# Kernel tuning notes

Measured on AMD Instinct MI355X. Metric: run time of the kernel, lower is better.

The kernel has to match this reference:

```python
import jax, jax.numpy as jnp
import numpy as np

EPS = 1e-7  # K.epsilon()
ROUTINGS = 3
NUM_CAPSULE = 32
DIM_CAPSULE = 64


def squash(x, axis=-1):
    # NOTE: faithful to the source: x / sqrt(sum(x^2) + eps) (no squash factor)
    s = jnp.sum(jnp.square(x), axis=axis, keepdims=True)
    return x / jnp.sqrt(s + EPS)


def setup_inputs() -> dict:
    key = jax.random.key(0)
    k1, k2 = jax.random.split(key)
    B, I, C = 32, 1024, 256
    u_vecs = jax.random.normal(k1, (B, I, C), dtype=jnp.float32)
    # glorot-ish scale for the capsule kernel (1x1 conv == matmul C -> N*D)
    W = jax.random.normal(k2, (C, NUM_CAPSULE * DIM_CAPSULE), dtype=jnp.float32) * 0.03
    return {"u_vecs": u_vecs, "W": W}


def reference(u_vecs, W):
    B, I, C = u_vecs.shape
    N, D = NUM_CAPSULE, DIM_CAPSULE
    # conv1d with kernel size 1 == matmul; reshape + permute to (B, N, I, D)
    u_hat = jnp.einsum('bic,ce->bie', u_vecs, W)  # (B, I, N*D)
    u_hat = u_hat.reshape(B, I, N, D).transpose(0, 2, 1, 3)  # (B, N, I, D)

    b = jnp.zeros((B, N, I), dtype=u_hat.dtype)
    outputs = None
    for i in range(ROUTINGS):
        c = jax.nn.softmax(b, axis=1)  # softmax over num_capsule axis
        outputs = squash(jnp.einsum('bni,bnid->bnd', c, u_hat))  # (B, N, D)
        if i < ROUTINGS - 1:
            b = jnp.einsum('bnd,bnid->bni', outputs, u_hat)
    return outputs
```

## Files before the change

### kernel.cpp

```cpp
#include <hip/hip_runtime.h>
#include <math.h>


constexpr int Bn = 32, In = 1024, Cn = 256, Nn = 32, Dn = 64, ND = 2048;

typedef __attribute__((ext_vector_type(8))) short bf16x8;
typedef __attribute__((ext_vector_type(4))) float f32x4;

__device__ __forceinline__ unsigned int packbf2(float a, float b) {
  unsigned int xa = __float_as_uint(a), xb = __float_as_uint(b);
  xa = (xa + 0x7fffu + ((xa >> 16) & 1u)) >> 16;
  xb = (xb + 0x7fffu + ((xb >> 16) & 1u)) >> 16;
  return xa | (xb << 16);
}
__device__ __forceinline__ unsigned short packbf1(float a) {
  unsigned int x = __float_as_uint(a);
  return (unsigned short)((x + 0x7fffu + ((x >> 16) & 1u)) >> 16);
}
__device__ __forceinline__ float bfu(unsigned short us) {
  return __uint_as_float((unsigned int)us << 16);
}

__global__ __launch_bounds__(256) void k_pre(
    const float* __restrict__ u, const float* __restrict__ W,
    float* __restrict__ psu, unsigned short* __restrict__ Wbf,
    unsigned short* __restrict__ WbfT, unsigned short* __restrict__ ub16,
    unsigned short* __restrict__ uT16) {
  const int z = blockIdx.x, tid = threadIdx.x;
  if (z < 1024) {
    int b = z >> 5, ch = z & 31;
    const float* up = u + ((size_t)(b * In + ch * 32)) * Cn + tid;
    unsigned short* ubp = ub16 + ((size_t)(b * In + ch * 32)) * Cn + tid;
    float s = 0.f;
    unsigned int q[16];
#pragma unroll
    for (int m = 0; m < 16; ++m) {
      float v0 = up[(size_t)(2 * m) * Cn];
      float v1 = up[(size_t)(2 * m + 1) * Cn];
      s += v0 + v1;
      ubp[(size_t)(2 * m) * Cn] = packbf1(v0);
      ubp[(size_t)(2 * m + 1) * Cn] = packbf1(v1);
      q[m] = packbf2(v0, v1);
    }
    psu[(size_t)z * Cn + tid] = s;
    unsigned short* tp = uT16 + ((size_t)(b * Cn + tid)) * In + ch * 32;
    *(uint4*)&tp[0]  = make_uint4(q[0], q[1], q[2], q[3]);
    *(uint4*)&tp[8]  = make_uint4(q[4], q[5], q[6], q[7]);
    *(uint4*)&tp[16] = make_uint4(q[8], q[9], q[10], q[11]);
    *(uint4*)&tp[24] = make_uint4(q[12], q[13], q[14], q[15]);
  } else if (z < 1152) {
    __shared__ float tile[64][65];
    int t = z - 1024;
    int x0 = (t & 31) * 64, y0 = (t >> 5) * 64;
    int lx = tid & 63, ly = tid >> 6;
#pragma unroll
    for (int k = 0; k < 16; ++k) {
      int y = ly + k * 4;
      tile[y][lx] = W[(size_t)(y0 + y) * ND + x0 + lx];
    }
    __syncthreads();
#pragma unroll
    for (int k = 0; k < 8; ++k) {
      int idx = tid + k * 256;
      int row = idx >> 5, cu = idx & 31;
      unsigned int v = packbf2(tile[2 * cu][row], tile[2 * cu + 1][row]);
      *(unsigned int*)&WbfT[(size_t)(x0 + row) * Cn + y0 + 2 * cu] = v;
    }
  } else {
    int zb = z - 1152;
    const float* src = W + (size_t)zb * 4096;
    unsigned short* dst = Wbf + (size_t)zb * 4096;
#pragma unroll
    for (int k = 0; k < 4; ++k) {
      int off = k * 1024 + tid * 4;
      const float4 v = *(const float4*)&src[off];
      *(uint2*)&dst[off] = make_uint2(packbf2(v.x, v.y), packbf2(v.z, v.w));
    }
  }
}

__global__ __launch_bounds__(512) void k_sst(
    const void* __restrict__ src, int srcBf16, long bS, long nS, long cS,
    float scale, const unsigned short* __restrict__ Wbf,
    const unsigned short* __restrict__ WbfT, unsigned short* __restrict__ tb,
    float* __restrict__ outp, int writeT) {
  int bn = blockIdx.x, b = bn >> 5, n = bn & 31;
  int tid = threadIdx.x;
  __shared__ float vs[Cn];
  __shared__ float ol[Dn];
  __shared__ float scr[4352];
  {
    const int g = tid >> 5, co = tid & 31;
    float acc[8];
#pragma unroll
    for (int e = 0; e < 8; ++e) acc[e] = 0.f;
    if (srcBf16) {
      const unsigned short* p =
          (const unsigned short*)src + b * bS + n * nS + co * 8;
#pragma unroll
      for (int k = 0; k < 2; ++k) {
        union { bf16x8 v; unsigned short us[8]; } w;
        w.v = *(const bf16x8*)&p[(size_t)(g * 2 + k) * cS];
#pragma unroll
        for (int e = 0; e < 8; ++e) acc[e] += bfu(w.us[e]);
      }
    } else {
      const float* p = (const float*)src + b * bS + n * nS + co * 8;
#pragma unroll
      for (int k = 0; k < 2; ++k) {
        const float4 v0 = *(const float4*)&p[(size_t)(g * 2 + k) * cS];
        const float4 v1 = *(const float4*)&p[(size_t)(g * 2 + k) * cS + 4];
        acc[0] += v0.x; acc[1] += v0.y; acc[2] += v0.z; acc[3] += v0.w;
        acc[4] += v1.x; acc[5] += v1.y; acc[6] += v1.z; acc[7] += v1.w;
      }
    }
    *(float4*)&scr[g * 272 + co * 8] =
        make_float4(acc[0], acc[1], acc[2], acc[3]);
    *(float4*)&scr[g * 272 + co * 8 + 4] =
        make_float4(acc[4], acc[5], acc[6], acc[7]);
  }
  __syncthreads();
  if (tid < 256) {
    float s = 0.f;
#pragma unroll
    for (int k = 0; k < 16; ++k) s += scr[k * 272 + tid];
    vs[tid] = s * scale;
  }
  __syncthreads();
  {
    const int cg = tid >> 3, do8 = tid & 7;
    const unsigned short* wp =
        Wbf + (size_t)(cg * 4) * ND + (size_t)n * Dn + do8 * 8;
    float acc[8];
#pragma unroll
    for (int e = 0; e < 8; ++e) acc[e] = 0.f;
#pragma unroll
    for (int j = 0; j < 4; ++j) {
      union { bf16x8 v; unsigned short us[8]; } w;
      w.v = *(const bf16x8*)&wp[(size_t)j * ND];
      const float vc = vs[cg * 4 + j];
#pragma unroll
      for (int e = 0; e < 8; ++e) acc[e] += vc * bfu(w.us[e]);
    }
    *(float4*)&scr[cg * 68 + do8 * 8] =
        make_float4(acc[0], acc[1], acc[2], acc[3]);
    *(float4*)&scr[cg * 68 + do8 * 8 + 4] =
        make_float4(acc[4], acc[5], acc[6], acc[7]);
  }
  __syncthreads();
  if (tid < 64) {
    float a = 0.f;
#pragma unroll
    for (int k = 0; k < 64; ++k) a += scr[k * 68 + tid];
    float sq = a * a;
#pragma unroll
    for (int off = 32; off > 0; off >>= 1) sq += __shfl_xor(sq, off, 64);
    float o = a / sqrtf(sq + 1e-7f);
    ol[tid] = o;
    if (outp) outp[(size_t)bn * Dn + tid] = o;
  }
  __syncthreads();
  if (writeT) {
    {
      const int dg = tid >> 5, co = tid & 31;
      const unsigned short* wt =
          WbfT + (size_t)(n * Dn + dg * 4) * Cn + co * 8;
      float acc[8];
#pragma unroll
      for (int e = 0; e < 8; ++e) acc[e] = 0.f;
#pragma unroll
      for (int e = 0; e < 4; ++e) {
        union { bf16x8 v; unsigned short us[8]; } w;
        w.v = *(const bf16x8*)&wt[(size_t)e * Cn];
        const float od = ol[dg * 4 + e];
#pragma unroll
        for (int cc = 0; cc < 8; ++cc) acc[cc] += od * bfu(w.us[cc]);
      }
      *(float4*)&scr[dg * 272 + co * 8] =
          make_float4(acc[0], acc[1], acc[2], acc[3]);
      *(float4*)&scr[dg * 272 + co * 8 + 4] =
          make_float4(acc[4], acc[5], acc[6], acc[7]);
    }
    __syncthreads();
    if (tid < 256) {
      float s = 0.f;
#pragma unroll
      for (int k = 0; k < 16; ++k) s += scr[k * 272 + tid];
      tb[(size_t)bn * Cn + tid] = packbf1(s);
    }
  }
}

__global__ __launch_bounds__(256, 4) void k_route(
    const unsigned short* __restrict__ tbb,
    const unsigned short* __restrict__ ub16,
    const unsigned short* __restrict__ uT16,
    unsigned short* __restrict__ pvb) {
  const int b = blockIdx.x, itile = blockIdx.y, i0 = itile * 32;
  const int tid = threadIdx.x;
  const int lane = tid & 63, w = tid >> 6;
  const int mrow = lane & 15, quad = lane >> 4;

  __shared__ unsigned short t_l[32][264];
  __shared__ unsigned short cm_l[32][40];
  __shared__ float bb_l[32][36];
  __shared__ float smr[2][8][32];

  {
    const unsigned short* tp = tbb + (size_t)b * Nn * Cn;
#pragma unroll
    for (int k = 0; k < 8; ++k) {
      int idx = tid + k * 256;
      int row = idx >> 6, q = idx & 63;
      *(uint2*)&t_l[row][q * 4] = *(const uint2*)&tp[(size_t)row * Cn + q * 4];
    }
  }
  __syncthreads();

  {
    const int i0t = (w & 1) * 16, n0t = (w >> 1) * 16;
    const unsigned short* ubp =
        ub16 + ((size_t)(b * In + i0 + i0t + mrow)) * Cn + quad * 8;
    f32x4 acc = {0.f, 0.f, 0.f, 0.f};
#pragma unroll
    for (int k0 = 0; k0 < 8; ++k0) {
      const bf16x8 af = *(const bf16x8*)(ubp + k0 * 32);
      const bf16x8 bf = *(const bf16x8*)&t_l[n0t + mrow][k0 * 32 + quad * 8];
      acc = __builtin_amdgcn_mfma_f32_16x16x32_bf16(af, bf, acc, 0, 0, 0);
    }
#pragma unroll
    for (int r = 0; r < 4; ++r)
      bb_l[n0t + mrow][i0t + quad * 4 + r] = acc[r];
  }
  __syncthreads();

  {
    const int i = tid & 31, g = tid >> 5;
    float m4 = fmaxf(fmaxf(bb_l[g * 4 + 0][i], bb_l[g * 4 + 1][i]),
                     fmaxf(bb_l[g * 4 + 2][i], bb_l[g * 4 + 3][i]));
    smr[0][g][i] = m4;
    __syncthreads();
    float m = smr[0][0][i];
#pragma unroll
    for (int k = 1; k < 8; ++k) m = fmaxf(m, smr[0][k][i]);
    float e[4];
    float s4 = 0.f;
#pragma unroll
    for (int r = 0; r < 4; ++r) {
      e[r] = __expf(bb_l[g * 4 + r][i] - m);
      s4 += e[r];
    }
    smr[1][g][i] = s4;
    __syncthreads();
    float ss = 0.f;
#pragma unroll
    for (int k = 0; k < 8; ++k) ss += smr[1][k][i];
    float inv = 1.f / ss;
#pragma unroll
    for (int r = 0; r < 4; ++r) cm_l[g * 4 + r][i] = packbf1(e[r] * inv);
  }
  __syncthreads();

  unsigned short* pvs = &t_l[0][0];
  {
    const int mt = w & 1;
    const bf16x8 af = *(const bf16x8*)&cm_l[mt * 16 + mrow][quad * 8];
    const unsigned short* utp =
        uT16 + ((size_t)(b * Cn + (w >> 1) * 128 + mrow)) * In + i0 + quad * 8;
#pragma unroll
    for (int j = 0; j < 8; ++j) {
      const int ct = (w >> 1) * 8 + j;
      const bf16x8 bfv = *(const bf16x8*)&utp[(size_t)(j * 16) * In];
      f32x4 d = {0.f, 0.f, 0.f, 0.f};
      d = __builtin_amdgcn_mfma_f32_16x16x32_bf16(af, bfv, d, 0, 0, 0);
#pragma unroll
      for (int r = 0; r < 4; ++r)
        pvs[(size_t)(mt * 16 + quad * 4 + r) * 264 + ct * 16 + mrow] =
            packbf1(d[r]);
    }
  }
  __syncthreads();
  {
    unsigned short* pb = pvb + (size_t)((b * 32 + itile) * Nn) * Cn;
    const int rg = tid >> 5, co = tid & 31;
#pragma unroll
    for (int k = 0; k < 4; ++k) {
      int row = rg + k * 8;
      const uint4 v = *(const uint4*)&pvs[(size_t)row * 264 + co * 8];
      *(uint4*)&pb[(size_t)row * Cn + co * 8] = v;
    }
  }
}

extern "C" void kernel_launch(void* const* d_in, const int* in_sizes, int n_in,
                              void* d_out, int out_size, void* d_ws, size_t ws_size,
                              hipStream_t stream) {
  (void)in_sizes; (void)n_in; (void)out_size; (void)ws_size;
  const float* u = (const float*)d_in[0];
  const float* W = (const float*)d_in[1];
  float* out = (float*)d_out;
  float* ws = (float*)d_ws;
  unsigned short* pvb  = (unsigned short*)ws;
  float*          psu  = ws + 4194304;
  unsigned short* Wbf  = (unsigned short*)(ws + 4456448);
  unsigned short* WbfT = (unsigned short*)(ws + 4718592);
  unsigned short* tb16 = (unsigned short*)(ws + 4980736);
  unsigned short* ub16 = (unsigned short*)(ws + 5242880);
  unsigned short* uT16 = (unsigned short*)(ws + 9437184);

  k_pre<<<1280, 256, 0, stream>>>(u, W, psu, Wbf, WbfT, ub16, uT16);
  k_sst<<<1024, 512, 0, stream>>>(psu, 0, 8192L, 0L, 256L, 1.0f / 32.0f,
                                  Wbf, WbfT, tb16, nullptr, 1);
  k_route<<<dim3(32, 32), 256, 0, stream>>>(tb16, ub16, uT16, pvb);
  k_sst<<<1024, 512, 0, stream>>>(pvb, 1, 262144L, 256L, 8192L, 1.0f,
                                  Wbf, WbfT, tb16, nullptr, 1);
  k_route<<<dim3(32, 32), 256, 0, stream>>>(tb16, ub16, uT16, pvb);
  k_sst<<<1024, 512, 0, stream>>>(pvb, 1, 262144L, 256L, 8192L, 1.0f,
                                  Wbf, WbfT, tb16, out, 0);
}
```

Measured before the change: 127.6 us.

## Process four batches per k_sst block to reuse W loads across batches

Each k_sst block now handles one capsule n for four batch rows instead of one, so every bf16 weight element loaded from Wbf and WbfT feeds four accumulators. The grid shrinks from 1024 to 256 blocks, and the thread mapping changes to scalar per-lane loads with wave-level partial sums staged in shared memory. This cuts weight traffic per output by a factor of four. In exchange it launches fewer blocks and uses narrower, non-vectorized global loads, which may lower occupancy and load efficiency on the source reduction.

```diff
diff --git a/kernel.cpp b/kernel.cpp
--- a/kernel.cpp
+++ b/kernel.cpp
@@ -84,109 +84,93 @@
     float scale, const unsigned short* __restrict__ Wbf,
     const unsigned short* __restrict__ WbfT, unsigned short* __restrict__ tb,
     float* __restrict__ outp, int writeT) {
-  int bn = blockIdx.x, b = bn >> 5, n = bn & 31;
-  int tid = threadIdx.x;
-  __shared__ float vs[Cn];
-  __shared__ float ol[Dn];
-  __shared__ float scr[4352];
-  {
-    const int g = tid >> 5, co = tid & 31;
-    float acc[8];
-#pragma unroll
-    for (int e = 0; e < 8; ++e) acc[e] = 0.f;
+  const int bx = blockIdx.x;
+  const int n = bx & 31, bg = bx >> 5;
+  const int tid = threadIdx.x;
+  const int wid = tid >> 6, lane = tid & 63;
+  __shared__ float vsh[4][256];
+  __shared__ float pw[8][4][64];
+  __shared__ float ol[4][64];
+  __shared__ float pt[2][4][256];
+
+  {
+    const int bb = tid >> 7, c0 = tid & 127;
+    const long base = (long)(bg * 4 + bb) * bS + (long)n * nS;
+    float a0 = 0.f, a1 = 0.f;
     if (srcBf16) {
-      const unsigned short* p =
-          (const unsigned short*)src + b * bS + n * nS + co * 8;
-#pragma unroll
-      for (int k = 0; k < 2; ++k) {
-        union { bf16x8 v; unsigned short us[8]; } w;
-        w.v = *(const bf16x8*)&p[(size_t)(g * 2 + k) * cS];
-#pragma unroll
-        for (int e = 0; e < 8; ++e) acc[e] += bfu(w.us[e]);
+      const unsigned short* p = (const unsigned short*)src + base;
+#pragma unroll
+      for (int it = 0; it < 32; ++it) {
+        a0 += bfu(p[(size_t)it * cS + c0]);
+        a1 += bfu(p[(size_t)it * cS + c0 + 128]);
       }
     } else {
-      const float* p = (const float*)src + b * bS + n * nS + co * 8;
-#pragma unroll
-      for (int k = 0; k < 2; ++k) {
-        const float4 v0 = *(const float4*)&p[(size_t)(g * 2 + k) * cS];
-        const float4 v1 = *(const float4*)&p[(size_t)(g * 2 + k) * cS + 4];
-        acc[0] += v0.x; acc[1] += v0.y; acc[2] += v0.z; acc[3] += v0.w;
-        acc[4] += v1.x; acc[5] += v1.y; acc[6] += v1.z; acc[7] += v1.w;
+      const float* p = (const float*)src + base;
+#pragma unroll
+      for (int it = 0; it < 32; ++it) {
+        a0 += p[(size_t)it * cS + c0];
+        a1 += p[(size_t)it * cS + c0 + 128];
       }
     }
-    *(float4*)&scr[g * 272 + co * 8] =
-        make_float4(acc[0], acc[1], acc[2], acc[3]);
-    *(float4*)&scr[g * 272 + co * 8 + 4] =
-        make_float4(acc[4], acc[5], acc[6], acc[7]);
+    vsh[bb][c0] = a0 * scale;
+    vsh[bb][c0 + 128] = a1 * scale;
+  }
+  __syncthreads();
+  {
+    const unsigned short* wp = Wbf + (size_t)(wid * 32) * ND + n * Dn + lane;
+    float a0 = 0.f, a1 = 0.f, a2 = 0.f, a3 = 0.f;
+#pragma unroll
+    for (int j = 0; j < 32; ++j) {
+      const float wval = bfu(wp[(size_t)j * ND]);
+      const int c = wid * 32 + j;
+      a0 += vsh[0][c] * wval;
+      a1 += vsh[1][c] * wval;
+      a2 += vsh[2][c] * wval;
+      a3 += vsh[3][c] * wval;
+    }
+    pw[wid][0][lane] = a0; pw[wid][1][lane] = a1;
+    pw[wid][2][lane] = a2; pw[wid][3][lane] = a3;
   }
   __syncthreads();
   if (tid < 256) {
-    float s = 0.f;
-#pragma unroll
-    for (int k = 0; k < 16; ++k) s += scr[k * 272 + tid];
-    vs[tid] = s * scale;
-  }
-  __syncthreads();
-  {
-    const int cg = tid >> 3, do8 = tid & 7;
-    const unsigned short* wp =
-        Wbf + (size_t)(cg * 4) * ND + (size_t)n * Dn + do8 * 8;
-    float acc[8];
-#pragma unroll
-    for (int e = 0; e < 8; ++e) acc[e] = 0.f;
-#pragma unroll
-    for (int j = 0; j < 4; ++j) {
-      union { bf16x8 v; unsigned short us[8]; } w;
-      w.v = *(const bf16x8*)&wp[(size_t)j * ND];
-      const float vc = vs[cg * 4 + j];
-#pragma unroll
-      for (int e = 0; e < 8; ++e) acc[e] += vc * bfu(w.us[e]);
-    }
-    *(float4*)&scr[cg * 68 + do8 * 8] =
-        make_float4(acc[0], acc[1], acc[2], acc[3]);
-    *(float4*)&scr[cg * 68 + do8 * 8 + 4] =
-        make_float4(acc[4], acc[5], acc[6], acc[7]);
-  }
-  __syncthreads();
-  if (tid < 64) {
+    const int bb = tid >> 6, d = tid & 63;
     float a = 0.f;
 #pragma unroll
-    for (int k = 0; k < 64; ++k) a += scr[k * 68 + tid];
+    for (int k = 0; k < 8; ++k) a += pw[k][bb][d];
     float sq = a * a;
 #pragma unroll
     for (int off = 32; off > 0; off >>= 1) sq += __shfl_xor(sq, off, 64);
     float o = a / sqrtf(sq + 1e-7f);
-    ol[tid] = o;
-    if (outp) outp[(size_t)bn * Dn + tid] = o;
+    ol[bb][d] = o;
+    if (outp) outp[(size_t)((bg * 4 + bb) * 32 + n) * 64 + d] = o;
   }
   __syncthreads();
   if (writeT) {
     {
-      const int dg = tid >> 5, co = tid & 31;
+      const int dg = tid >> 8, c = tid & 255;
       const unsigned short* wt =
-          WbfT + (size_t)(n * Dn + dg * 4) * Cn + co * 8;
-      float acc[8];
-#pragma unroll
-      for (int e = 0; e < 8; ++e) acc[e] = 0.f;
-#pragma unroll
-      for (int e = 0; e < 4; ++e) {
-        union { bf16x8 v; unsigned short us[8]; } w;
-        w.v = *(const bf16x8*)&wt[(size_t)e * Cn];
-        const float od = ol[dg * 4 + e];
-#pragma unroll
-        for (int cc = 0; cc < 8; ++cc) acc[cc] += od * bfu(w.us[cc]);
+          WbfT + (size_t)(n * Dn + dg * 32) * Cn + c;
+      float a0 = 0.f, a1 = 0.f, a2 = 0.f, a3 = 0.f;
+#pragma unroll
+      for (int d2 = 0; d2 < 32; ++d2) {
+        const float wval = bfu(wt[(size_t)d2 * Cn]);
+        const int d = dg * 32 + d2;
+        a0 += ol[0][d] * wval;
+        a1 += ol[1][d] * wval;
+        a2 += ol[2][d] * wval;
+        a3 += ol[3][d] * wval;
       }
-      *(float4*)&scr[dg * 272 + co * 8] =
-          make_float4(acc[0], acc[1], acc[2], acc[3]);
-      *(float4*)&scr[dg * 272 + co * 8 + 4] =
-          make_float4(acc[4], acc[5], acc[6], acc[7]);
+      pt[dg][0][c] = a0; pt[dg][1][c] = a1;
+      pt[dg][2][c] = a2; pt[dg][3][c] = a3;
     }
     __syncthreads();
     if (tid < 256) {
-      float s = 0.f;
-#pragma unroll
-      for (int k = 0; k < 16; ++k) s += scr[k * 272 + tid];
-      tb[(size_t)bn * Cn + tid] = packbf1(s);
+      const int c = tid;
+#pragma unroll
+      for (int bb = 0; bb < 4; ++bb) {
+        float t = pt[0][bb][c] + pt[1][bb][c];
+        tb[(size_t)((bg * 4 + bb) * 32 + n) * Cn + c] = packbf1(t);
+      }
     }
   }
 }
@@ -309,12 +293,12 @@
   unsigned short* uT16 = (unsigned short*)(ws + 9437184);
 
   k_pre<<<1280, 256, 0, stream>>>(u, W, psu, Wbf, WbfT, ub16, uT16);
-  k_sst<<<1024, 512, 0, stream>>>(psu, 0, 8192L, 0L, 256L, 1.0f / 32.0f,
-                                  Wbf, WbfT, tb16, nullptr, 1);
+  k_sst<<<256, 512, 0, stream>>>(psu, 0, 8192L, 0L, 256L, 1.0f / 32.0f,
+                                 Wbf, WbfT, tb16, nullptr, 1);
   k_route<<<dim3(32, 32), 256, 0, stream>>>(tb16, ub16, uT16, pvb);
-  k_sst<<<1024, 512, 0, stream>>>(pvb, 1, 262144L, 256L, 8192L, 1.0f,
-                                  Wbf, WbfT, tb16, nullptr, 1);
+  k_sst<<<256, 512, 0, stream>>>(pvb, 1, 262144L, 256L, 8192L, 1.0f,
+                                 Wbf, WbfT, tb16, nullptr, 1);
   k_route<<<dim3(32, 32), 256, 0, stream>>>(tb16, ub16, uT16, pvb);
-  k_sst<<<1024, 512, 0, stream>>>(pvb, 1, 262144L, 256L, 8192L, 1.0f,
-                                  Wbf, WbfT, tb16, out, 0);
-}
+  k_sst<<<256, 512, 0, stream>>>(pvb, 1, 262144L, 256L, 8192L, 1.0f,
+                                 Wbf, WbfT, tb16, out, 0);
+}
```

Result: no change. 126.9 us, median of 2 (-0.6%).
